# Performance work log

Hardware: AMD Instinct MI355X
Metric: run time of the kernel (lower is better)

The kernel has to match this reference:

```python
import jax, jax.numpy as jnp
import numpy as np

NUM_HEADS = 16


def setup_inputs() -> dict:
    key = jax.random.key(0)
    ks = jax.random.split(key, 6)
    B, S, D = 2, 2048, 1024
    hidden_states = jax.random.normal(ks[0], (B, S, D), dtype=jnp.float32)
    attention_mask = jnp.zeros((B, 1, 1, S), dtype=jnp.float32)  # additive mask
    # Linear weights stored as [in, out] (equivalent to torch weight.T)
    W_qkv = jax.random.normal(ks[1], (D, 3 * D), dtype=jnp.float32) * (1.0 / np.sqrt(D))
    b_qkv = jnp.zeros((3 * D,), dtype=jnp.float32)
    W_proj = jax.random.normal(ks[2], (D, D), dtype=jnp.float32) * (1.0 / np.sqrt(D))
    b_proj = jnp.zeros((D,), dtype=jnp.float32)
    return {
        "hidden_states": hidden_states,
        "attention_mask": attention_mask,
        "W_qkv": W_qkv,
        "b_qkv": b_qkv,
        "W_proj": W_proj,
        "b_proj": b_proj,
    }


def reference(hidden_states, attention_mask, W_qkv, b_qkv, W_proj, b_proj):
    B, S, D = hidden_states.shape
    H = NUM_HEADS
    hd = D // H
    scale = 1.0 / jnp.sqrt(jnp.asarray(hd, hidden_states.dtype))

    qkv = hidden_states @ W_qkv + b_qkv            # [B,S,3D]
    q, k, v = jnp.split(qkv, 3, axis=-1)
    # [B,S,D] -> [B,H,S,hd]
    split_heads = lambda t: t.reshape(B, S, H, hd).transpose(0, 2, 1, 3)
    q, k, v = split_heads(q), split_heads(k), split_heads(v)

    scores = jnp.einsum("bhqd,bhkd->bhqk", q, k) * scale + attention_mask
    attn = jax.nn.softmax(scores, axis=-1)
    ctx = jnp.einsum("bhqk,bhkd->bhqd", attn, v)   # [B,H,S,hd]
    ctx = ctx.transpose(0, 2, 1, 3).reshape(B, S, D)
    return ctx @ W_proj + b_proj
```

## Files before the change

kernel.cpp:

```cpp
#include <hip/hip_runtime.h>
#include <hip/hip_bf16.h>

typedef short short8 __attribute__((ext_vector_type(8)));
typedef float floatx4 __attribute__((ext_vector_type(4)));
typedef int intx4 __attribute__((ext_vector_type(4)));
typedef int intx2 __attribute__((ext_vector_type(2)));

#define S_LEN 2048
#define DMODEL 1024
#define NH 16
#define HD 64
#define BATCH 2

static __device__ __forceinline__ short f2bf(float x) {
    __hip_bfloat16 h = __float2bfloat16(x);
    return *(short*)&h;
}

static __device__ __forceinline__ unsigned pk2(float lo, float hi) {
    unsigned a = (unsigned)(unsigned short)f2bf(lo);
    unsigned b = (unsigned)(unsigned short)f2bf(hi);
    return a | (b << 16);
}

static __device__ __forceinline__ void async_ld16(const __hip_bfloat16* g, __hip_bfloat16* l) {
    __builtin_amdgcn_global_load_lds(
        (const __attribute__((address_space(1))) unsigned int*)g,
        (__attribute__((address_space(3))) unsigned int*)l, 16, 0, 0);
}

__global__ __launch_bounds__(256) void cvt_kernel(const float* __restrict__ X,
                                                  __hip_bfloat16* __restrict__ Y) {
    int i = (blockIdx.x * 256 + threadIdx.x) * 8;
    floatx4 f0 = *(const floatx4*)&X[i];
    floatx4 f1 = *(const floatx4*)&X[i + 4];
    short8 s;
    s[0] = f2bf(f0[0]); s[1] = f2bf(f0[1]); s[2] = f2bf(f0[2]); s[3] = f2bf(f0[3]);
    s[4] = f2bf(f1[0]); s[5] = f2bf(f1[1]); s[6] = f2bf(f1[2]); s[7] = f2bf(f1[3]);
    *(short8*)&Y[i] = s;
}

__global__ void transpose_kernel(const float* __restrict__ W,
                                 __hip_bfloat16* __restrict__ Wt, int K, int N) {
    __shared__ float tile[32][33];
    int n0 = blockIdx.x * 32, k0 = blockIdx.y * 32;
    int tx = threadIdx.x, ty = threadIdx.y;
#pragma unroll
    for (int i = 0; i < 32; i += 8)
        tile[ty + i][tx] = W[(size_t)(k0 + ty + i) * N + n0 + tx];
    __syncthreads();
#pragma unroll
    for (int i = 0; i < 32; i += 8)
        Wt[(size_t)(n0 + ty + i) * K + k0 + tx] = __float2bfloat16(tile[tx][ty + i]);
}

__global__ __launch_bounds__(256) void gemm128(
    const __hip_bfloat16* __restrict__ A, const __hip_bfloat16* __restrict__ Bt,
    const float* __restrict__ bias, float* __restrict__ Cf,
    __hip_bfloat16* __restrict__ Qp, __hip_bfloat16* __restrict__ Kp,
    __hip_bfloat16* __restrict__ Vt, int M, int N, int K, int mode) {
    __shared__ __align__(16) __hip_bfloat16 As[2][128 * 32];
    __shared__ __align__(16) __hip_bfloat16 Bs[2][128 * 32];
    const int gx = gridDim.x, gy = gridDim.y;
    const int flat = blockIdx.y * gx + blockIdx.x;
    const int cpx = (gx * gy) >> 3;
    const int id2 = (flat & 7) * cpx + (flat >> 3);
    const int m0 = (id2 % gy) * 128, n0 = (id2 / gy) * 128;
    const int t = threadIdx.x;
    const int wave = t >> 6, lane = t & 63;
    const int quad = lane >> 4, m16 = lane & 15;
    const int wm = (wave >> 1) * 64, wn = (wave & 1) * 64;
    const int srow = lane >> 2, scol = (lane & 3) * 8;

    const int rb0 = wave * 32, rb1 = wave * 32 + 16;
    const size_t aoff0 = (size_t)(m0 + rb0 + srow) * K + scol;
    const size_t aoff1 = (size_t)(m0 + rb1 + srow) * K + scol;
    const size_t boff0 = (size_t)(n0 + rb0 + srow) * K + scol;
    const size_t boff1 = (size_t)(n0 + rb1 + srow) * K + scol;

    async_ld16(&A[aoff0], &As[0][rb0 * 32]);
    async_ld16(&A[aoff1], &As[0][rb1 * 32]);
    async_ld16(&Bt[boff0], &Bs[0][rb0 * 32]);
    async_ld16(&Bt[boff1], &Bs[0][rb1 * 32]);
    __syncthreads();

    floatx4 acc[4][4] = {};
    const int NI = K >> 5;
    for (int it = 0; it < NI; ++it) {
        const int cur = it & 1;
        if (it < NI - 1) {
            const int k0 = (it + 1) * 32;
            async_ld16(&A[aoff0 + k0], &As[cur ^ 1][rb0 * 32]);
            async_ld16(&A[aoff1 + k0], &As[cur ^ 1][rb1 * 32]);
            async_ld16(&Bt[boff0 + k0], &Bs[cur ^ 1][rb0 * 32]);
            async_ld16(&Bt[boff1 + k0], &Bs[cur ^ 1][rb1 * 32]);
        }
        short8 af[4], bfr[4];
#pragma unroll
        for (int i = 0; i < 4; i++)
            af[i] = *(const short8*)&As[cur][(wm + i * 16 + m16) * 32 + quad * 8];
#pragma unroll
        for (int j = 0; j < 4; j++)
            bfr[j] = *(const short8*)&Bs[cur][(wn + j * 16 + m16) * 32 + quad * 8];
#pragma unroll
        for (int i = 0; i < 4; i++)
#pragma unroll
            for (int j = 0; j < 4; j++)
                acc[i][j] = __builtin_amdgcn_mfma_f32_16x16x32_bf16(af[i], bfr[j], acc[i][j], 0, 0, 0);
        __syncthreads();
    }
    if (mode == 0) {
#pragma unroll
        for (int i = 0; i < 4; i++)
#pragma unroll
            for (int j = 0; j < 4; j++) {
                int col = n0 + wn + j * 16 + m16;
                float bv = bias[col];
#pragma unroll
                for (int r = 0; r < 4; r++) {
                    int row = m0 + wm + i * 16 + quad * 4 + r;
                    Cf[(size_t)row * N + col] = acc[i][j][r] + bv;
                }
            }
    } else if (n0 < 2 * DMODEL) {
#pragma unroll
        for (int i = 0; i < 4; i++)
#pragma unroll
            for (int j = 0; j < 4; j++) {
                int col = n0 + wn + j * 16 + m16;
                float bv = bias[col];
#pragma unroll
                for (int r = 0; r < 4; r++) {
                    int row = m0 + wm + i * 16 + quad * 4 + r;
                    __hip_bfloat16 hv = __float2bfloat16(acc[i][j][r] + bv);
                    int tt = col >> 10, rem = col & 1023;
                    int h = rem >> 6, d = rem & 63;
                    int b = row >> 11, s = row & 2047;
                    if (tt == 0) Qp[((size_t)(b * NH + h) * S_LEN + s) * HD + d] = hv;
                    else         Kp[((size_t)(b * NH + h) * S_LEN + s) * HD + d] = hv;
                }
            }
    } else {
        char* T = (char*)As;
        const int bq = m0 >> 11;
        const int s_base = m0 & 2047;
        for (int p = 0; p < 4; p++) {
            if (wave == p) {
#pragma unroll
                for (int j = 0; j < 4; j++) {
                    const int drow = j * 16 + m16;
                    const float bv = bias[n0 + wn + j * 16 + m16];
                    const int within = (quad & 1) * 4;
#pragma unroll
                    for (int i = 0; i < 4; i++) {
                        const int colc = i * 2 + (quad >> 1);
                        const int physc = colc ^ (drow & 7);
                        intx2 v;
                        v[0] = (int)pk2(acc[i][j][0] + bv, acc[i][j][1] + bv);
                        v[1] = (int)pk2(acc[i][j][2] + bv, acc[i][j][3] + bv);
                        *(intx2*)(T + drow * 128 + physc * 16 + within * 2) = v;
                    }
                }
            }
            __syncthreads();
            {
                const int dl = t >> 2;
                const int sseg = (t & 3) * 16;
                const int c0 = (sseg >> 3) ^ (dl & 7);
                const int c1 = ((sseg >> 3) + 1) ^ (dl & 7);
                short8 a0 = *(const short8*)(T + dl * 128 + c0 * 16);
                short8 a1 = *(const short8*)(T + dl * 128 + c1 * 16);
                const int hh = (n0 - 2 * DMODEL + (p & 1) * 64) >> 6;
                const int sg = s_base + (p >> 1) * 64 + sseg;
                __hip_bfloat16* dst = &Vt[((size_t)(bq * NH + hh) * HD + dl) * S_LEN + sg];
                *(short8*)dst = a0;
                *(short8*)(dst + 8) = a1;
            }
            __syncthreads();
        }
    }
}

__global__ __launch_bounds__(256) void gemm64(
    const __hip_bfloat16* __restrict__ A, const __hip_bfloat16* __restrict__ Bt,
    const float* __restrict__ bias, float* __restrict__ Cf, int M, int N, int K) {
    __shared__ __align__(16) __hip_bfloat16 As[2][64 * 32];
    __shared__ __align__(16) __hip_bfloat16 Bs[2][64 * 32];
    const int gx = gridDim.x, gy = gridDim.y;
    const int flat = blockIdx.y * gx + blockIdx.x;
    const int cpx = (gx * gy) >> 3;
    const int id2 = (flat & 7) * cpx + (flat >> 3);
    const int m0 = (id2 % gy) * 64, n0 = (id2 / gy) * 64;
    const int t = threadIdx.x;
    const int wave = t >> 6, lane = t & 63;
    const int quad = lane >> 4, m16 = lane & 15;
    const int srow = lane >> 2, scol = (lane & 3) * 8;

    const int rb = wave * 16;
    const size_t aoff = (size_t)(m0 + rb + srow) * K + scol;
    const size_t boff = (size_t)(n0 + rb + srow) * K + scol;

    async_ld16(&A[aoff], &As[0][rb * 32]);
    async_ld16(&Bt[boff], &Bs[0][rb * 32]);
    __syncthreads();

    floatx4 acc[4] = {};
    const int NI = K >> 5;
    for (int it = 0; it < NI; ++it) {
        const int cur = it & 1;
        if (it < NI - 1) {
            const int k0 = (it + 1) * 32;
            async_ld16(&A[aoff + k0], &As[cur ^ 1][rb * 32]);
            async_ld16(&Bt[boff + k0], &Bs[cur ^ 1][rb * 32]);
        }
        short8 af[4];
#pragma unroll
        for (int i = 0; i < 4; i++)
            af[i] = *(const short8*)&As[cur][(i * 16 + m16) * 32 + quad * 8];
        short8 bfr = *(const short8*)&Bs[cur][(wave * 16 + m16) * 32 + quad * 8];
#pragma unroll
        for (int i = 0; i < 4; i++)
            acc[i] = __builtin_amdgcn_mfma_f32_16x16x32_bf16(af[i], bfr, acc[i], 0, 0, 0);
        __syncthreads();
    }
    {
        const int col = n0 + wave * 16 + m16;
        const float bv = bias[col];
#pragma unroll
        for (int i = 0; i < 4; i++)
#pragma unroll
            for (int r = 0; r < 4; r++) {
                int row = m0 + i * 16 + quad * 4 + r;
                Cf[(size_t)row * N + col] = acc[i][r] + bv;
            }
    }
}

__global__ __launch_bounds__(512, 8) void attn_kernel(
    const __hip_bfloat16* __restrict__ Q,
    const __hip_bfloat16* __restrict__ K,
    const __hip_bfloat16* __restrict__ Vt,
    const float* __restrict__ mask,
    __hip_bfloat16* __restrict__ ctx) {
    __shared__ __align__(16) __hip_bfloat16 smem[16384];
    __shared__ float wsm[S_LEN];
    const int bh = blockIdx.x;
    const int b = bh >> 4, h = bh & 15;
    const int t = threadIdx.x, wave = t >> 6, lane = t & 63;
    const int team = wave >> 2, tw = wave & 3;
    const int quad = lane >> 4, m16 = lane & 15;
    const int qbase = blockIdx.y * 64 + tw * 16;
    const int ko = team * (S_LEN / 2);
    const __hip_bfloat16* Qh = Q + (size_t)bh * S_LEN * HD;
    const __hip_bfloat16* Kh = K + (size_t)bh * S_LEN * HD;
    const __hip_bfloat16* Vh = Vt + (size_t)bh * HD * S_LEN;
    const float* mb = mask + (size_t)b * S_LEN;
    const float LOG2E = 1.44269504f;
    const float scale2 = 0.125f * LOG2E;
    const float M_FIX2 = 20.0f * LOG2E;

    __hip_bfloat16* Ksb = smem + team * 8192;
    __hip_bfloat16* Vsb = smem + team * 8192 + 4096;

    {
        floatx4 mv = *(const floatx4*)&mb[t * 4];
        floatx4 wv;
#pragma unroll
        for (int r = 0; r < 4; r++) wv[r] = __builtin_fmaf(mv[r], LOG2E, -M_FIX2);
        *(floatx4*)&wsm[t * 4] = wv;
    }

    const int kr = lane >> 3, kc = lane & 7;
    const int kgoff = (tw * 8 + kr) * HD + ((kc ^ kr) * 8);
    const int vr = lane >> 2, vc = lane & 3;
    const int vd = tw * 16 + vr;
    const int vgoff = vd * S_LEN + (((vc ^ ((vd >> 1) & 3))) * 8);
    __hip_bfloat16* kdst0 = Ksb + tw * 512;
    __hip_bfloat16* kdst1 = Ksb + 2048 + tw * 512;
    __hip_bfloat16* vdst0 = Vsb + tw * 512;
    __hip_bfloat16* vdst1 = Vsb + 2048 + tw * 512;

    short8 aq0 = *(const short8*)&Qh[(size_t)(qbase + m16) * HD + quad * 8];
    short8 aq1 = *(const short8*)&Qh[(size_t)(qbase + m16) * HD + 32 + quad * 8];

    const short ONEB = (short)0x3F80;
    const short8 ones = {ONEB, ONEB, ONEB, ONEB, ONEB, ONEB, ONEB, ONEB};

    async_ld16(&Kh[(size_t)ko * HD + kgoff], kdst0);
    async_ld16(&Vh[(size_t)ko + vgoff], vdst0);
    __syncthreads();

    floatx4 o[4] = {};
    floatx4 lacc = {};
    const int swk = m16 & 7;
    const int e = quad & 1;
    const int C = ((quad & 1) << 1) | (quad >> 1);
    const int vsl = (C ^ ((m16 >> 1) & 3)) * 8;

    const int NIT = (S_LEN / 2) / 32;
    for (int it = 0; it < NIT; it++) {
        const int k0 = it * 32;
        const int cur = it & 1;
        if (it < NIT - 1) {
            async_ld16(&Kh[(size_t)(ko + k0 + 32) * HD + kgoff], cur ? kdst0 : kdst1);
            async_ld16(&Vh[(size_t)(ko + k0 + 32) + vgoff], cur ? vdst0 : vdst1);
        }

        const __hip_bfloat16* Kc = Ksb + cur * 2048;
        floatx4 sc[2] = {};
        __builtin_amdgcn_s_setprio(1);
#pragma unroll
        for (int kt = 0; kt < 2; kt++) {
            const int row = kt * 16 + m16;
            short8 ak0 = *(const short8*)&Kc[row * 64 + ((quad ^ swk) * 8)];
            short8 ak1 = *(const short8*)&Kc[row * 64 + (((quad + 4) ^ swk) * 8)];
            sc[kt] = __builtin_amdgcn_mfma_f32_16x16x32_bf16(ak0, aq0, sc[kt], 0, 0, 0);
            sc[kt] = __builtin_amdgcn_mfma_f32_16x16x32_bf16(ak1, aq1, sc[kt], 0, 0, 0);
        }
        __builtin_amdgcn_s_setprio(0);

        unsigned dk[2][2];
#pragma unroll
        for (int kt = 0; kt < 2; kt++) {
            floatx4 wv = *(const floatx4*)&wsm[ko + k0 + kt * 16 + quad * 4];
            float p0 = __builtin_amdgcn_exp2f(__builtin_fmaf(sc[kt][0], scale2, wv[0]));
            float p1 = __builtin_amdgcn_exp2f(__builtin_fmaf(sc[kt][1], scale2, wv[1]));
            float p2 = __builtin_amdgcn_exp2f(__builtin_fmaf(sc[kt][2], scale2, wv[2]));
            float p3 = __builtin_amdgcn_exp2f(__builtin_fmaf(sc[kt][3], scale2, wv[3]));
            dk[kt][0] = pk2(p0, p1);
            dk[kt][1] = pk2(p2, p3);
        }

        unsigned s0 = e ? dk[0][0] : dk[1][0];
        unsigned s1 = e ? dk[0][1] : dk[1][1];
        unsigned r0 = (unsigned)__builtin_amdgcn_ds_swizzle((int)s0, 0x401F);
        unsigned r1 = (unsigned)__builtin_amdgcn_ds_swizzle((int)s1, 0x401F);
        intx4 wa;
        wa[0] = (int)(e ? r0 : dk[0][0]);
        wa[1] = (int)(e ? r1 : dk[0][1]);
        wa[2] = (int)(e ? dk[1][0] : r0);
        wa[3] = (int)(e ? dk[1][1] : r1);
        short8 ap = *(short8*)&wa;

        const __hip_bfloat16* Vc = Vsb + cur * 2048;
        __builtin_amdgcn_s_setprio(1);
        lacc = __builtin_amdgcn_mfma_f32_16x16x32_bf16(ap, ones, lacc, 0, 0, 0);
#pragma unroll
        for (int tt = 0; tt < 4; tt++) {
            const int d = tt * 16 + m16;
            short8 bv = *(const short8*)&Vc[d * 32 + vsl];
            o[tt] = __builtin_amdgcn_mfma_f32_16x16x32_bf16(ap, bv, o[tt], 0, 0, 0);
        }
        __builtin_amdgcn_s_setprio(0);
        __syncthreads();
    }

    float* xch = (float*)smem;
    const int xi = (tw * 64 + lane) * 21;
    if (team == 1) {
#pragma unroll
        for (int tt = 0; tt < 4; tt++)
#pragma unroll
            for (int r = 0; r < 4; r++) xch[xi + tt * 4 + r] = o[tt][r];
#pragma unroll
        for (int r = 0; r < 4; r++) xch[xi + 16 + r] = lacc[r];
    }
    __syncthreads();
    if (team == 0) {
        float li[4];
#pragma unroll
        for (int r = 0; r < 4; r++) li[r] = 1.0f / (lacc[r] + xch[xi + 16 + r]);
#pragma unroll
        for (int tt = 0; tt < 4; tt++)
#pragma unroll
            for (int r = 0; r < 4; r++) {
                int srow = qbase + quad * 4 + r;
                int d = tt * 16 + m16;
                float v = (o[tt][r] + xch[xi + tt * 4 + r]) * li[r];
                ctx[((size_t)b * S_LEN + srow) * DMODEL + h * HD + d] = __float2bfloat16(v);
            }
    }
}

extern "C" void kernel_launch(void* const* d_in, const int* in_sizes, int n_in,
                              void* d_out, int out_size, void* d_ws, size_t ws_size,
                              hipStream_t stream) {
    (void)in_sizes; (void)n_in; (void)out_size; (void)ws_size;
    const float* hidden = (const float*)d_in[0];
    const float* mask   = (const float*)d_in[1];
    const float* Wqkv   = (const float*)d_in[2];
    const float* bqkv   = (const float*)d_in[3];
    const float* Wproj  = (const float*)d_in[4];
    const float* bproj  = (const float*)d_in[5];
    float* out = (float*)d_out;

    __hip_bfloat16* ws = (__hip_bfloat16*)d_ws;
    const size_t Q4 = 4u * 1024 * 1024;
    __hip_bfloat16* Qp      = ws;
    __hip_bfloat16* Kp      = ws + 1 * Q4;
    __hip_bfloat16* Vt      = ws + 2 * Q4;
    __hip_bfloat16* hid_bf  = ws + 3 * Q4;
    __hip_bfloat16* ctx     = ws + 3 * Q4;
    __hip_bfloat16* Wqkv_t  = ws + 4 * Q4;
    __hip_bfloat16* Wproj_t = ws + 4 * Q4;

    cvt_kernel<<<dim3(4 * 1024 * 1024 / 2048), 256, 0, stream>>>(hidden, hid_bf);
    transpose_kernel<<<dim3(3072 / 32, 1024 / 32), dim3(32, 8), 0, stream>>>(Wqkv, Wqkv_t, 1024, 3072);

    gemm128<<<dim3(3072 / 128, 4096 / 128), 256, 0, stream>>>(
        hid_bf, Wqkv_t, bqkv, nullptr, Qp, Kp, Vt, BATCH * S_LEN, 3 * DMODEL, DMODEL, 1);

    transpose_kernel<<<dim3(1024 / 32, 1024 / 32), dim3(32, 8), 0, stream>>>(Wproj, Wproj_t, 1024, 1024);

    attn_kernel<<<dim3(BATCH * NH, S_LEN / 64), 512, 0, stream>>>(Qp, Kp, Vt, mask, ctx);

    gemm64<<<dim3(1024 / 64, 4096 / 64), 256, 0, stream>>>(
        ctx, Wproj_t, bproj, out, BATCH * S_LEN, DMODEL, DMODEL);
}
```

Measured before the change: 214.7 us.

## Triple-buffer GEMM shared-memory tiles with partial vmcnt waits

Both projection GEMM kernels move from double to triple buffering of the A/B shared-memory tiles, prefetching two K-steps ahead. Full __syncthreads is replaced by an explicit s_waitcnt vmcnt(N) that waits only for the oldest outstanding loads, followed by a raw barrier. The aim is to keep more global loads in flight and hide memory latency behind the MFMA work. In exchange it uses 50% more LDS, which may lower occupancy, and it relies on precise vmcnt counting of the async loads for correctness.

After: 216.7 us. Within noise of the previous version (+0.9%).

```diff
diff --git a/kernel.cpp b/kernel.cpp
--- a/kernel.cpp
+++ b/kernel.cpp
@@ -59,8 +59,8 @@
     const float* __restrict__ bias, float* __restrict__ Cf,
     __hip_bfloat16* __restrict__ Qp, __hip_bfloat16* __restrict__ Kp,
     __hip_bfloat16* __restrict__ Vt, int M, int N, int K, int mode) {
-    __shared__ __align__(16) __hip_bfloat16 As[2][128 * 32];
-    __shared__ __align__(16) __hip_bfloat16 Bs[2][128 * 32];
+    __shared__ __align__(16) __hip_bfloat16 As[3][128 * 32];
+    __shared__ __align__(16) __hip_bfloat16 Bs[3][128 * 32];
     const int gx = gridDim.x, gy = gridDim.y;
     const int flat = blockIdx.y * gx + blockIdx.x;
     const int cpx = (gx * gy) >> 3;
@@ -78,22 +78,33 @@
     const size_t boff0 = (size_t)(n0 + rb0 + srow) * K + scol;
     const size_t boff1 = (size_t)(n0 + rb1 + srow) * K + scol;
 
+    const int NI = K >> 5;
     async_ld16(&A[aoff0], &As[0][rb0 * 32]);
     async_ld16(&A[aoff1], &As[0][rb1 * 32]);
     async_ld16(&Bt[boff0], &Bs[0][rb0 * 32]);
     async_ld16(&Bt[boff1], &Bs[0][rb1 * 32]);
-    __syncthreads();
+    if (NI > 1) {
+        async_ld16(&A[aoff0 + 32], &As[1][rb0 * 32]);
+        async_ld16(&A[aoff1 + 32], &As[1][rb1 * 32]);
+        async_ld16(&Bt[boff0 + 32], &Bs[1][rb0 * 32]);
+        async_ld16(&Bt[boff1 + 32], &Bs[1][rb1 * 32]);
+        asm volatile("s_waitcnt vmcnt(4)" ::: "memory");
+    } else {
+        asm volatile("s_waitcnt vmcnt(0)" ::: "memory");
+    }
+    __builtin_amdgcn_s_barrier();
+    __builtin_amdgcn_sched_barrier(0);
 
     floatx4 acc[4][4] = {};
-    const int NI = K >> 5;
     for (int it = 0; it < NI; ++it) {
-        const int cur = it & 1;
-        if (it < NI - 1) {
-            const int k0 = (it + 1) * 32;
-            async_ld16(&A[aoff0 + k0], &As[cur ^ 1][rb0 * 32]);
-            async_ld16(&A[aoff1 + k0], &As[cur ^ 1][rb1 * 32]);
-            async_ld16(&Bt[boff0 + k0], &Bs[cur ^ 1][rb0 * 32]);
-            async_ld16(&Bt[boff1 + k0], &Bs[cur ^ 1][rb1 * 32]);
+        const int cur = it % 3;
+        if (it + 2 < NI) {
+            const int k0 = (it + 2) * 32;
+            const int nb = (it + 2) % 3;
+            async_ld16(&A[aoff0 + k0], &As[nb][rb0 * 32]);
+            async_ld16(&A[aoff1 + k0], &As[nb][rb1 * 32]);
+            async_ld16(&Bt[boff0 + k0], &Bs[nb][rb0 * 32]);
+            async_ld16(&Bt[boff1 + k0], &Bs[nb][rb1 * 32]);
         }
         short8 af[4], bfr[4];
 #pragma unroll
@@ -107,7 +118,10 @@
 #pragma unroll
             for (int j = 0; j < 4; j++)
                 acc[i][j] = __builtin_amdgcn_mfma_f32_16x16x32_bf16(af[i], bfr[j], acc[i][j], 0, 0, 0);
-        __syncthreads();
+        if (it + 2 < NI) asm volatile("s_waitcnt vmcnt(4)" ::: "memory");
+        else             asm volatile("s_waitcnt vmcnt(0)" ::: "memory");
+        __builtin_amdgcn_s_barrier();
+        __builtin_amdgcn_sched_barrier(0);
     }
     if (mode == 0) {
 #pragma unroll
@@ -184,8 +198,8 @@
 __global__ __launch_bounds__(256) void gemm64(
     const __hip_bfloat16* __restrict__ A, const __hip_bfloat16* __restrict__ Bt,
     const float* __restrict__ bias, float* __restrict__ Cf, int M, int N, int K) {
-    __shared__ __align__(16) __hip_bfloat16 As[2][64 * 32];
-    __shared__ __align__(16) __hip_bfloat16 Bs[2][64 * 32];
+    __shared__ __align__(16) __hip_bfloat16 As[3][64 * 32];
+    __shared__ __align__(16) __hip_bfloat16 Bs[3][64 * 32];
     const int gx = gridDim.x, gy = gridDim.y;
     const int flat = blockIdx.y * gx + blockIdx.x;
     const int cpx = (gx * gy) >> 3;
@@ -200,18 +214,27 @@
     const size_t aoff = (size_t)(m0 + rb + srow) * K + scol;
     const size_t boff = (size_t)(n0 + rb + srow) * K + scol;
 
+    const int NI = K >> 5;
     async_ld16(&A[aoff], &As[0][rb * 32]);
     async_ld16(&Bt[boff], &Bs[0][rb * 32]);
-    __syncthreads();
+    if (NI > 1) {
+        async_ld16(&A[aoff + 32], &As[1][rb * 32]);
+        async_ld16(&Bt[boff + 32], &Bs[1][rb * 32]);
+        asm volatile("s_waitcnt vmcnt(2)" ::: "memory");
+    } else {
+        asm volatile("s_waitcnt vmcnt(0)" ::: "memory");
+    }
+    __builtin_amdgcn_s_barrier();
+    __builtin_amdgcn_sched_barrier(0);
 
     floatx4 acc[4] = {};
-    const int NI = K >> 5;
     for (int it = 0; it < NI; ++it) {
-        const int cur = it & 1;
-        if (it < NI - 1) {
-            const int k0 = (it + 1) * 32;
-            async_ld16(&A[aoff + k0], &As[cur ^ 1][rb * 32]);
-            async_ld16(&Bt[boff + k0], &Bs[cur ^ 1][rb * 32]);
+        const int cur = it % 3;
+        if (it + 2 < NI) {
+            const int k0 = (it + 2) * 32;
+            const int nb = (it + 2) % 3;
+            async_ld16(&A[aoff + k0], &As[nb][rb * 32]);
+            async_ld16(&Bt[boff + k0], &Bs[nb][rb * 32]);
         }
         short8 af[4];
 #pragma unroll
@@ -221,7 +244,10 @@
 #pragma unroll
         for (int i = 0; i < 4; i++)
             acc[i] = __builtin_amdgcn_mfma_f32_16x16x32_bf16(af[i], bfr, acc[i], 0, 0, 0);
-        __syncthreads();
+        if (it + 2 < NI) asm volatile("s_waitcnt vmcnt(2)" ::: "memory");
+        else             asm volatile("s_waitcnt vmcnt(0)" ::: "memory");
+        __builtin_amdgcn_s_barrier();
+        __builtin_amdgcn_sched_barrier(0);
     }
     {
         const int col = n0 + wave * 16 + m16;
```
